# Performance work log

Hardware: AMD Instinct MI355X
Metric: run time of the kernel (lower is better)

The kernel has to match this reference:

```python
import jax, jax.numpy as jnp
import numpy as np

L, Q = 200, 21          # alignment length, number of Potts states (20 AAs + gap)
REG_H, REG_J = 0.01, 0.01  # L2 regularization strengths (reg_h, reg_J)
M = 1024                # number of sequences in the MSA


def setup_inputs() -> dict:
    key = jax.random.key(0)
    ks = jax.random.split(key, 6)
    X_tokens = jax.random.randint(ks[0], (M, L), 0, Q)
    weights = jax.random.uniform(ks[1], (M,), dtype=jnp.float32)
    fi = jax.random.uniform(ks[2], (L, Q), dtype=jnp.float32)
    fi_target = fi / fi.sum(axis=1, keepdims=True)  # single-site frequencies
    fij = jax.random.uniform(ks[3], (L, Q, L, Q), dtype=jnp.float32)
    fij_target = fij / fij.sum(axis=(1, 3), keepdims=True)  # pairwise frequencies
    h = jax.random.normal(ks[4], (L, Q), dtype=jnp.float32) * 1e-4
    J = jax.random.normal(ks[5], (L, Q, L, Q), dtype=jnp.float32) * 1e-4
    # remove_autocorr: zero self-couplings J[i,:,i,:]
    eye = jnp.eye(L, dtype=jnp.float32)[:, None, :, None]
    J = J * (1.0 - eye)
    return {"X_tokens": X_tokens, "weights": weights, "fi_target": fi_target,
            "fij_target": fij_target, "h": h, "J": J}


def _loss_third(X, weights, fi_target, fij_target, h, J):
    # loss_third_fn: sites i in [2L//3, L)
    start = 2 * L // 3
    w = weights / weights.sum()
    sites = jnp.arange(start, L)                         # (S,)
    causal = (jnp.arange(L)[None, :] < sites[:, None])   # (S, L), j < i mask
    Jm = J[start:] * causal[:, None, :, None].astype(J.dtype)  # (S, q, L, q)
    # energy_i = fi[i] @ h[i] + sum_{j<i} J[i,:,j,:] * fij[i,:,j,:], summed over i
    energy = (jnp.einsum('ia,ia->', fi_target[start:], h[start:])
              + jnp.einsum('iajb,iajb->', Jm, fij_target[start:]))
    # logits[n,i,a] = h[i,a] + sum_{j<i,b} J[i,a,j,b] * X[n,j,b]
    logits = jnp.einsum('njb,iajb->nia', X, Jm) + h[start:][None]  # (M, S, q)
    logZ = jax.scipy.special.logsumexp(logits, axis=-1)            # (M, S)
    nll = -(energy - jnp.einsum('ni,n->', logZ, w))
    loss = nll + REG_H * jnp.sum(h * h) + REG_J * jnp.sum(J * J)
    return loss, nll


def reference(X_tokens, weights, fi_target, fij_target, h, J):
    X = jax.nn.one_hot(X_tokens, Q, dtype=jnp.float32)  # (M, L, q)
    return _loss_third(X, weights, fi_target, fij_target, h, J)
```

## Files before the change

### kernel.cpp

```cpp
#include <hip/hip_runtime.h>
#include <cstdint>

#define LL    200
#define QQ    21
#define MM    1024
#define START 133
#define NS    67
#define RGH   0.01f
#define RGJ   0.01f

#define SLOT_J2  0
#define SLOT_E   64
#define SLOT_LZ  128
#define TOKT_OFF 1024
#define TOKT_BYTES ((size_t)LL * MM * 4)
#define SLAB_OFF (TOKT_OFF + TOKT_BYTES)
#define SLAB_BYTES ((size_t)2 * NS * QQ * MM * 4)
#define WS_FULL (SLAB_OFF + SLAB_BYTES)
#define WS_TOK  SLAB_OFF

#define TJ 12
#define PLANE 256
#define TILE_FLOATS (QQ * PLANE)

#define NB_P1 (NS * 8)
#define NB_JS 1024

typedef const uint32_t __attribute__((address_space(1)))* gq_t;
typedef uint32_t __attribute__((address_space(3)))* lq_t;

__device__ __forceinline__ float block_reduce_sum_256(float v) {
  __shared__ float sm[4];
  #pragma unroll
  for (int off = 32; off > 0; off >>= 1) v += __shfl_down(v, off, 64);
  const int lane = threadIdx.x & 63;
  const int wv   = threadIdx.x >> 6;
  __syncthreads();
  if (lane == 0) sm[wv] = v;
  __syncthreads();
  float r = 0.0f;
  if (threadIdx.x == 0) r = sm[0] + sm[1] + sm[2] + sm[3];
  return r;
}

__device__ __forceinline__ void dma_tile(
    const float* __restrict__ Ji, int j0, int rem, int wv, int lane,
    float* __restrict__ tile) {
  const int nlanes = (rem * QQ + 3) >> 2;
  if (lane < nlanes) {
    for (int a = wv; a < QQ; a += 4) {
      const float* g = Ji + a * (LL * QQ) + j0 * QQ + lane * 4;
      __builtin_amdgcn_global_load_lds((gq_t)g, (lq_t)(tile + a * PLANE),
                                       16, 0, 0);
    }
  }
}

__device__ __forceinline__ void tok_load(
    const int* __restrict__ tokT, const int* __restrict__ Xtok, int useT,
    int j0, int jend, int n, int (&bo)[TJ]) {
  #pragma unroll
  for (int k = 0; k < TJ; ++k) {
    if (j0 + k < jend) {
      const int j = j0 + k;
      const int b = useT ? tokT[j * MM + n] : Xtok[n * LL + j];
      bo[k] = k * QQ + b;
    }
  }
}

__device__ __forceinline__ void gather_tile(
    const float* __restrict__ tile, const int (&bo)[TJ], int rem,
    float (&lg)[QQ]) {
  #pragma unroll
  for (int jl = 0; jl < TJ; ++jl) {
    if (jl >= rem) break;
    const float* p = tile + bo[jl];
    #pragma unroll
    for (int a = 0; a < QQ; ++a) lg[a] += p[a * PLANE];
  }
}

template <bool MONO>
__device__ __forceinline__ void logz_body(
    const float* __restrict__ J, const int* __restrict__ tokT,
    const int* __restrict__ Xtok, int useT, const float* __restrict__ h,
    const float* __restrict__ w, float* __restrict__ slab,
    float* __restrict__ acc, int iI, int y, int z,
    float (*lds)[TILE_FLOATS]) {
  const int i  = START + iI;
  const int h0 = i >> 1;
  const int jbeg = MONO ? 0 : (y ? h0 : 0);
  const int jend = MONO ? i : (y ? i : h0);
  const int t = threadIdx.x, lane = t & 63, wv = t >> 6;
  const int n = z * 256 + t;
  const float* Ji = J + (size_t)i * (QQ * LL * QQ);
  const int ntiles = (jend - jbeg + TJ - 1) / TJ;

  float lg[QQ];
  #pragma unroll
  for (int a = 0; a < QQ; ++a) lg[a] = 0.0f;
  int boc[TJ], bon[TJ];

  dma_tile(Ji, jbeg, min(TJ, jend - jbeg), wv, lane, lds[0]);
  tok_load(tokT, Xtok, useT, jbeg, jend, n, boc);
  __syncthreads();

  for (int s = 0; s < ntiles; ++s) {
    const int j0  = jbeg + s * TJ;
    const int rem = min(TJ, jend - j0);
    const bool more = (s + 1 < ntiles);
    if (more) {
      const int j1 = j0 + TJ;
      dma_tile(Ji, j1, min(TJ, jend - j1), wv, lane, lds[(s + 1) & 1]);
      tok_load(tokT, Xtok, useT, j1, jend, n, bon);
    }
    gather_tile(lds[s & 1], boc, rem, lg);
    if (more) {
      #pragma unroll
      for (int k = 0; k < TJ; ++k) boc[k] = bon[k];
    }
    __syncthreads();
  }

  if (MONO) {
    const float* hi = h + i * QQ;
    float mx = -3.0e38f;
    #pragma unroll
    for (int a = 0; a < QQ; ++a) { lg[a] += hi[a]; mx = fmaxf(mx, lg[a]); }
    float sme = 0.0f;
    #pragma unroll
    for (int a = 0; a < QQ; ++a) sme += expf(lg[a] - mx);
    const float contrib = w[n] * (mx + logf(sme));
    const float tot = block_reduce_sum_256(contrib);
    if (t == 0) atomicAdd(acc + SLOT_LZ + (iI & 63), tot);
  } else {
    float* dst = slab + (((size_t)y * NS + iI) * QQ) * MM + n;
    #pragma unroll
    for (int a = 0; a < QQ; ++a) dst[a * MM] = lg[a];
  }
}

__device__ __forceinline__ void jsum_body(
    const float* __restrict__ J, const float* __restrict__ fij,
    float* __restrict__ acc, int jb) {
  const int t = threadIdx.x;
  const float4* __restrict__ J4 = (const float4*)J;
  float j2 = 0.0f;
  for (int f = jb * 256 + t; f < (LL * QQ * LL * QQ / 4); f += NB_JS * 256) {
    const float4 v = J4[f];
    j2 += v.x * v.x + v.y * v.y + v.z * v.z + v.w * v.w;
  }
  float e = 0.0f;
  for (int r = jb; r < NS * QQ; r += NB_JS) {
    const int iI = r / QQ;
    const int a  = r - iI * QQ;
    const int i  = START + iI;
    const size_t base = (size_t)i * (QQ * LL * QQ) + (size_t)a * (LL * QQ);
    const float4* __restrict__ Jb = (const float4*)(J + base);
    const float4* __restrict__ Fb = (const float4*)(fij + base);
    const int lim  = i * QQ;
    const int lim4 = lim >> 2;
    for (int f = t; f < lim4; f += 256) {
      const float4 v = Jb[f], u = Fb[f];
      e += v.x * u.x + v.y * u.y + v.z * u.z + v.w * u.w;
    }
    const int rem = lim & 3;
    if (t < rem) {
      const int p = lim4 * 4 + t;
      e += (J + base)[p] * (fij + base)[p];
    }
  }
  const float tj2 = block_reduce_sum_256(j2);
  const float te  = block_reduce_sum_256(e);
  if (t == 0) {
    atomicAdd(acc + SLOT_J2 + (jb & 63), tj2);
    atomicAdd(acc + SLOT_E  + (jb & 63), te);
  }
}

__global__ __launch_bounds__(256) void kern_mega(
    const float* __restrict__ J, const float* __restrict__ fij,
    const int* __restrict__ tokT, float* __restrict__ slab,
    float* __restrict__ acc) {
  __shared__ float lds[2][TILE_FLOATS];
  const int bx = blockIdx.x;
  if (bx < NB_P1) {
    const int iI  = bx % NS;
    const int sub = bx / NS;
    logz_body<false>(J, tokT, nullptr, 1, nullptr, nullptr, slab, acc,
                     iI, sub & 1, sub >> 1, lds);
  } else {
    jsum_body(J, fij, acc, bx - NB_P1);
  }
}

__global__ __launch_bounds__(256) void kern_logz_mono(
    const float* __restrict__ J, const int* __restrict__ tokT,
    const int* __restrict__ Xtok, int useT, const float* __restrict__ h,
    const float* __restrict__ w, float* __restrict__ acc) {
  __shared__ float lds[2][TILE_FLOATS];
  logz_body<true>(J, tokT, Xtok, useT, h, w, nullptr, acc,
                  blockIdx.x, 0, blockIdx.z, lds);
}

__global__ __launch_bounds__(256) void kern_jsum(
    const float* __restrict__ J, const float* __restrict__ fij,
    float* __restrict__ acc) {
  jsum_body(J, fij, acc, blockIdx.x);
}

__global__ __launch_bounds__(128) void kern_logz_p2(
    const float* __restrict__ slab, const float* __restrict__ h,
    const float* __restrict__ w, float* __restrict__ acc) {
  const int iI = blockIdx.x;
  const int n  = blockIdx.y * 128 + threadIdx.x;
  const float* s0 = slab + ((size_t)iI * QQ) * MM + n;
  const float* s1 = slab + (((size_t)NS + iI) * QQ) * MM + n;
  const float* hi = h + (START + iI) * QQ;
  float lg[QQ];
  float mx = -3.0e38f;
  #pragma unroll
  for (int a = 0; a < QQ; ++a) {
    lg[a] = s0[a * MM] + s1[a * MM] + hi[a];
    mx = fmaxf(mx, lg[a]);
  }
  float sme = 0.0f;
  #pragma unroll
  for (int a = 0; a < QQ; ++a) sme += expf(lg[a] - mx);
  float v = w[n] * (mx + logf(sme));
  #pragma unroll
  for (int off = 32; off > 0; off >>= 1) v += __shfl_down(v, off, 64);
  __shared__ float sm[2];
  if ((threadIdx.x & 63) == 0) sm[threadIdx.x >> 6] = v;
  __syncthreads();
  if (threadIdx.x == 0)
    atomicAdd(acc + SLOT_LZ + (blockIdx.x & 63), sm[0] + sm[1]);
}

__global__ __launch_bounds__(256) void kern_tokT(
    const int* __restrict__ X, int* __restrict__ tokT) {
  const int idx = blockIdx.x * 256 + threadIdx.x;
  if (idx < LL * MM) {
    const int j = idx / MM;
    const int n = idx - j * MM;
    tokT[idx] = X[n * LL + j];
  }
}

__global__ __launch_bounds__(256) void kern_final(
    const float* __restrict__ h, const float* __restrict__ fi,
    const float* __restrict__ w, const float* __restrict__ acc,
    float* __restrict__ out) {
  const int t = threadIdx.x;
  const float sj2 = block_reduce_sum_256(t < 64 ? acc[SLOT_J2 + t] : 0.0f);
  const float se  = block_reduce_sum_256(t < 64 ? acc[SLOT_E + t] : 0.0f);
  const float slz = block_reduce_sum_256(t < 64 ? acc[SLOT_LZ + t] : 0.0f);
  float hs = 0.0f, eh = 0.0f, ws = 0.0f;
  for (int idx = t; idx < LL * QQ; idx += 256) {
    const float hv = h[idx];
    hs += hv * hv;
    if (idx >= START * QQ) eh += fi[idx] * hv;
  }
  for (int idx = t; idx < MM; idx += 256) ws += w[idx];
  const float ths = block_reduce_sum_256(hs);
  const float teh = block_reduce_sum_256(eh);
  const float tws = block_reduce_sum_256(ws);
  if (t == 0) {
    const float energy = teh + se;
    const float nll = slz / tws - energy;
    out[0] = nll + RGH * ths + RGJ * sj2;
    out[1] = nll;
  }
}

extern "C" void kernel_launch(void* const* d_in, const int* in_sizes, int n_in,
                              void* d_out, int out_size, void* d_ws, size_t ws_size,
                              hipStream_t stream) {
  const int*   Xtok = (const int*)  d_in[0];
  const float* wts  = (const float*)d_in[1];
  const float* fi   = (const float*)d_in[2];
  const float* fij  = (const float*)d_in[3];
  const float* h    = (const float*)d_in[4];
  const float* J    = (const float*)d_in[5];
  float* out  = (float*)d_out;
  float* acc  = (float*)d_ws;
  int*   tokT = (int*)((char*)d_ws + TOKT_OFF);
  float* slab = (float*)((char*)d_ws + SLAB_OFF);

  hipMemsetAsync(d_ws, 0, 1024, stream);
  if (ws_size >= WS_FULL) {
    kern_tokT<<<(LL * MM + 255) / 256, 256, 0, stream>>>(Xtok, tokT);
    kern_mega<<<NB_P1 + NB_JS, 256, 0, stream>>>(J, fij, tokT, slab, acc);
    kern_logz_p2<<<dim3(NS, 8), 128, 0, stream>>>(slab, h, wts, acc);
    kern_final<<<1, 256, 0, stream>>>(h, fi, wts, acc, out);
  } else if (ws_size >= WS_TOK) {
    kern_tokT<<<(LL * MM + 255) / 256, 256, 0, stream>>>(Xtok, tokT);
    kern_jsum<<<NB_JS, 256, 0, stream>>>(J, fij, acc);
    kern_logz_mono<<<dim3(NS, 1, 4), 256, 0, stream>>>(J, tokT, Xtok, 1, h, wts, acc);
    kern_final<<<1, 256, 0, stream>>>(h, fi, wts, acc, out);
  } else {
    kern_jsum<<<NB_JS, 256, 0, stream>>>(J, fij, acc);
    kern_logz_mono<<<dim3(NS, 1, 4), 256, 0, stream>>>(J, nullptr, Xtok, 0, h, wts, acc);
    kern_final<<<1, 256, 0, stream>>>(h, fi, wts, acc, out);
  }
}
```

Measured before the change: 207.0 us.

## Fuse pipeline into persistent cooperative kernel with atomic work queue

Replaces the memset plus four separate launches with one cooperative persistent kernel. Inside it, blocks zero the accumulators and transpose the tokens, then pull logits and J-sum work units from an atomic counter, with the longest rows scheduled first; grid syncs separate this from the logsumexp reduction and the final reduction. It also shrinks the LDS tile (TJ 12 to 10, plane stride 256 to 212), makes the J² sweep read contiguous chunks per block, and widens the p2 blocks to 256 threads. The aim is to remove launch gaps and tail imbalance, at the cost of grid-wide sync overhead and a fixed grid size derived from the occupancy query.

```diff
diff --git a/kernel.cpp b/kernel.cpp
--- a/kernel.cpp
+++ b/kernel.cpp
@@ -1,5 +1,8 @@
 #include <hip/hip_runtime.h>
+#include <hip/hip_cooperative_groups.h>
 #include <cstdint>
+
+namespace cg = cooperative_groups;
 
 #define LL    200
 #define QQ    21
@@ -12,6 +15,7 @@
 #define SLOT_J2  0
 #define SLOT_E   64
 #define SLOT_LZ  128
+#define CTR_OFF  192
 #define TOKT_OFF 1024
 #define TOKT_BYTES ((size_t)LL * MM * 4)
 #define SLAB_OFF (TOKT_OFF + TOKT_BYTES)
@@ -19,12 +23,15 @@
 #define WS_FULL (SLAB_OFF + SLAB_BYTES)
 #define WS_TOK  SLAB_OFF
 
-#define TJ 12
-#define PLANE 256
+#define TJ 10
+#define PLANE 212
 #define TILE_FLOATS (QQ * PLANE)
 
-#define NB_P1 (NS * 8)
-#define NB_JS 1024
+#define NP1  (NS * 8)
+#define NJS  1024
+#define NTOT (NP1 + NJS)
+#define TOTAL4 (LL * QQ * LL * QQ / 4)
+#define CHUNK4 ((TOTAL4 + NJS - 1) / NJS)
 
 typedef const uint32_t __attribute__((address_space(1)))* gq_t;
 typedef uint32_t __attribute__((address_space(3)))* lq_t;
@@ -57,15 +64,10 @@
 }
 
 __device__ __forceinline__ void tok_load(
-    const int* __restrict__ tokT, const int* __restrict__ Xtok, int useT,
-    int j0, int jend, int n, int (&bo)[TJ]) {
+    const int* __restrict__ tokT, int j0, int jend, int n, int (&bo)[TJ]) {
   #pragma unroll
   for (int k = 0; k < TJ; ++k) {
-    if (j0 + k < jend) {
-      const int j = j0 + k;
-      const int b = useT ? tokT[j * MM + n] : Xtok[n * LL + j];
-      bo[k] = k * QQ + b;
-    }
+    if (j0 + k < jend) bo[k] = k * QQ + tokT[(j0 + k) * MM + n];
   }
 }
 
@@ -81,17 +83,14 @@
   }
 }
 
-template <bool MONO>
-__device__ __forceinline__ void logz_body(
+__device__ void p1_unit(
     const float* __restrict__ J, const int* __restrict__ tokT,
-    const int* __restrict__ Xtok, int useT, const float* __restrict__ h,
-    const float* __restrict__ w, float* __restrict__ slab,
-    float* __restrict__ acc, int iI, int y, int z,
+    float* __restrict__ slab, int iI, int y, int z,
     float (*lds)[TILE_FLOATS]) {
   const int i  = START + iI;
   const int h0 = i >> 1;
-  const int jbeg = MONO ? 0 : (y ? h0 : 0);
-  const int jend = MONO ? i : (y ? i : h0);
+  const int jbeg = y ? h0 : 0;
+  const int jend = y ? i : h0;
   const int t = threadIdx.x, lane = t & 63, wv = t >> 6;
   const int n = z * 256 + t;
   const float* Ji = J + (size_t)i * (QQ * LL * QQ);
@@ -103,7 +102,7 @@
   int boc[TJ], bon[TJ];
 
   dma_tile(Ji, jbeg, min(TJ, jend - jbeg), wv, lane, lds[0]);
-  tok_load(tokT, Xtok, useT, jbeg, jend, n, boc);
+  tok_load(tokT, jbeg, jend, n, boc);
   __syncthreads();
 
   for (int s = 0; s < ntiles; ++s) {
@@ -113,7 +112,7 @@
     if (more) {
       const int j1 = j0 + TJ;
       dma_tile(Ji, j1, min(TJ, jend - j1), wv, lane, lds[(s + 1) & 1]);
-      tok_load(tokT, Xtok, useT, j1, jend, n, bon);
+      tok_load(tokT, j1, jend, n, bon);
     }
     gather_tile(lds[s & 1], boc, rem, lg);
     if (more) {
@@ -123,36 +122,25 @@
     __syncthreads();
   }
 
-  if (MONO) {
-    const float* hi = h + i * QQ;
-    float mx = -3.0e38f;
-    #pragma unroll
-    for (int a = 0; a < QQ; ++a) { lg[a] += hi[a]; mx = fmaxf(mx, lg[a]); }
-    float sme = 0.0f;
-    #pragma unroll
-    for (int a = 0; a < QQ; ++a) sme += expf(lg[a] - mx);
-    const float contrib = w[n] * (mx + logf(sme));
-    const float tot = block_reduce_sum_256(contrib);
-    if (t == 0) atomicAdd(acc + SLOT_LZ + (iI & 63), tot);
-  } else {
-    float* dst = slab + (((size_t)y * NS + iI) * QQ) * MM + n;
-    #pragma unroll
-    for (int a = 0; a < QQ; ++a) dst[a * MM] = lg[a];
-  }
-}
-
-__device__ __forceinline__ void jsum_body(
+  float* dst = slab + (((size_t)y * NS + iI) * QQ) * MM + n;
+  #pragma unroll
+  for (int a = 0; a < QQ; ++a) dst[a * MM] = lg[a];
+}
+
+__device__ void jsum_unit(
     const float* __restrict__ J, const float* __restrict__ fij,
-    float* __restrict__ acc, int jb) {
+    float* __restrict__ acc, int v) {
   const int t = threadIdx.x;
   const float4* __restrict__ J4 = (const float4*)J;
   float j2 = 0.0f;
-  for (int f = jb * 256 + t; f < (LL * QQ * LL * QQ / 4); f += NB_JS * 256) {
-    const float4 v = J4[f];
-    j2 += v.x * v.x + v.y * v.y + v.z * v.z + v.w * v.w;
+  const int beg = v * CHUNK4;
+  const int end = min(beg + CHUNK4, TOTAL4);
+  for (int f = beg + t; f < end; f += 256) {
+    const float4 q = J4[f];
+    j2 += q.x * q.x + q.y * q.y + q.z * q.z + q.w * q.w;
   }
   float e = 0.0f;
-  for (int r = jb; r < NS * QQ; r += NB_JS) {
+  for (int r = v; r < NS * QQ; r += NJS) {
     const int iI = r / QQ;
     const int a  = r - iI * QQ;
     const int i  = START + iI;
@@ -162,8 +150,8 @@
     const int lim  = i * QQ;
     const int lim4 = lim >> 2;
     for (int f = t; f < lim4; f += 256) {
-      const float4 v = Jb[f], u = Fb[f];
-      e += v.x * u.x + v.y * u.y + v.z * u.z + v.w * u.w;
+      const float4 q = Jb[f], u = Fb[f];
+      e += q.x * u.x + q.y * u.y + q.z * u.z + q.w * u.w;
     }
     const int rem = lim & 3;
     if (t < rem) {
@@ -174,47 +162,16 @@
   const float tj2 = block_reduce_sum_256(j2);
   const float te  = block_reduce_sum_256(e);
   if (t == 0) {
-    atomicAdd(acc + SLOT_J2 + (jb & 63), tj2);
-    atomicAdd(acc + SLOT_E  + (jb & 63), te);
-  }
-}
-
-__global__ __launch_bounds__(256) void kern_mega(
-    const float* __restrict__ J, const float* __restrict__ fij,
-    const int* __restrict__ tokT, float* __restrict__ slab,
-    float* __restrict__ acc) {
-  __shared__ float lds[2][TILE_FLOATS];
-  const int bx = blockIdx.x;
-  if (bx < NB_P1) {
-    const int iI  = bx % NS;
-    const int sub = bx / NS;
-    logz_body<false>(J, tokT, nullptr, 1, nullptr, nullptr, slab, acc,
-                     iI, sub & 1, sub >> 1, lds);
-  } else {
-    jsum_body(J, fij, acc, bx - NB_P1);
-  }
-}
-
-__global__ __launch_bounds__(256) void kern_logz_mono(
-    const float* __restrict__ J, const int* __restrict__ tokT,
-    const int* __restrict__ Xtok, int useT, const float* __restrict__ h,
-    const float* __restrict__ w, float* __restrict__ acc) {
-  __shared__ float lds[2][TILE_FLOATS];
-  logz_body<true>(J, tokT, Xtok, useT, h, w, nullptr, acc,
-                  blockIdx.x, 0, blockIdx.z, lds);
-}
-
-__global__ __launch_bounds__(256) void kern_jsum(
-    const float* __restrict__ J, const float* __restrict__ fij,
-    float* __restrict__ acc) {
-  jsum_body(J, fij, acc, blockIdx.x);
-}
-
-__global__ __launch_bounds__(128) void kern_logz_p2(
+    atomicAdd(acc + SLOT_J2 + (v & 63), tj2);
+    atomicAdd(acc + SLOT_E  + (v & 63), te);
+  }
+}
+
+__device__ void p2_unit(
     const float* __restrict__ slab, const float* __restrict__ h,
-    const float* __restrict__ w, float* __restrict__ acc) {
-  const int iI = blockIdx.x;
-  const int n  = blockIdx.y * 128 + threadIdx.x;
+    const float* __restrict__ w, float* __restrict__ acc, int iI, int z) {
+  const int t = threadIdx.x;
+  const int n = z * 256 + t;
   const float* s0 = slab + ((size_t)iI * QQ) * MM + n;
   const float* s1 = slab + (((size_t)NS + iI) * QQ) * MM + n;
   const float* hi = h + (START + iI) * QQ;
@@ -228,27 +185,12 @@
   float sme = 0.0f;
   #pragma unroll
   for (int a = 0; a < QQ; ++a) sme += expf(lg[a] - mx);
-  float v = w[n] * (mx + logf(sme));
-  #pragma unroll
-  for (int off = 32; off > 0; off >>= 1) v += __shfl_down(v, off, 64);
-  __shared__ float sm[2];
-  if ((threadIdx.x & 63) == 0) sm[threadIdx.x >> 6] = v;
-  __syncthreads();
-  if (threadIdx.x == 0)
-    atomicAdd(acc + SLOT_LZ + (blockIdx.x & 63), sm[0] + sm[1]);
-}
-
-__global__ __launch_bounds__(256) void kern_tokT(
-    const int* __restrict__ X, int* __restrict__ tokT) {
-  const int idx = blockIdx.x * 256 + threadIdx.x;
-  if (idx < LL * MM) {
-    const int j = idx / MM;
-    const int n = idx - j * MM;
-    tokT[idx] = X[n * LL + j];
-  }
-}
-
-__global__ __launch_bounds__(256) void kern_final(
+  const float contrib = w[n] * (mx + logf(sme));
+  const float tot = block_reduce_sum_256(contrib);
+  if (t == 0) atomicAdd(acc + SLOT_LZ + (iI & 63), tot);
+}
+
+__device__ void final_body(
     const float* __restrict__ h, const float* __restrict__ fi,
     const float* __restrict__ w, const float* __restrict__ acc,
     float* __restrict__ out) {
@@ -272,6 +214,135 @@
     out[0] = nll + RGH * ths + RGJ * sj2;
     out[1] = nll;
   }
+}
+
+__global__ __launch_bounds__(256) void kern_coop(
+    const int* __restrict__ Xtok, const float* __restrict__ wts,
+    const float* __restrict__ fi, const float* __restrict__ fij,
+    const float* __restrict__ h, const float* __restrict__ J,
+    float* __restrict__ acc, int* __restrict__ tokT,
+    float* __restrict__ slab, float* __restrict__ out) {
+  __shared__ float lds[2][TILE_FLOATS];
+  __shared__ int s_unit;
+  cg::grid_group grid = cg::this_grid();
+  const int t = threadIdx.x;
+  const int nb = gridDim.x;
+
+  if (blockIdx.x == 0) acc[t] = 0.0f;
+  for (int idx = blockIdx.x * 256 + t; idx < LL * MM; idx += nb * 256) {
+    const int j = idx >> 10;
+    const int n = idx & (MM - 1);
+    tokT[idx] = Xtok[n * LL + j];
+  }
+  __threadfence();
+  grid.sync();
+
+  int* ctr = (int*)(acc + CTR_OFF);
+  for (;;) {
+    __syncthreads();
+    if (t == 0) s_unit = atomicAdd(ctr, 1);
+    __syncthreads();
+    const int u = s_unit;
+    if (u >= NTOT) break;
+    if (u < NP1) {
+      const int s    = u % NS;
+      const int rest = u / NS;
+      p1_unit(J, tokT, slab, NS - 1 - s, rest & 1, rest >> 1, lds);
+    } else {
+      jsum_unit(J, fij, acc, u - NP1);
+    }
+  }
+  __threadfence();
+  grid.sync();
+
+  for (int u = blockIdx.x; u < NS * 4; u += nb) {
+    p2_unit(slab, h, wts, acc, u >> 2, u & 3);
+  }
+  __threadfence();
+  grid.sync();
+
+  if (blockIdx.x == 0) final_body(h, fi, wts, acc, out);
+}
+
+__global__ __launch_bounds__(256) void kern_tokT(
+    const int* __restrict__ X, int* __restrict__ tokT) {
+  const int idx = blockIdx.x * 256 + threadIdx.x;
+  if (idx < LL * MM) tokT[idx] = X[(idx & (MM - 1)) * LL + (idx >> 10)];
+}
+
+__global__ __launch_bounds__(256) void kern_mega(
+    const float* __restrict__ J, const float* __restrict__ fij,
+    const int* __restrict__ tokT, float* __restrict__ slab,
+    float* __restrict__ acc) {
+  __shared__ float lds[2][TILE_FLOATS];
+  const int bx = blockIdx.x;
+  if (bx < NP1) {
+    const int s    = bx % NS;
+    const int rest = bx / NS;
+    p1_unit(J, tokT, slab, NS - 1 - s, rest & 1, rest >> 1, lds);
+  } else {
+    jsum_unit(J, fij, acc, bx - NP1);
+  }
+}
+
+__global__ __launch_bounds__(256) void kern_logz_p2(
+    const float* __restrict__ slab, const float* __restrict__ h,
+    const float* __restrict__ w, float* __restrict__ acc) {
+  p2_unit(slab, h, w, acc, blockIdx.x, blockIdx.y);
+}
+
+__global__ __launch_bounds__(256) void kern_final(
+    const float* __restrict__ h, const float* __restrict__ fi,
+    const float* __restrict__ w, const float* __restrict__ acc,
+    float* __restrict__ out) {
+  final_body(h, fi, w, acc, out);
+}
+
+__global__ __launch_bounds__(256) void kern_logz_mono(
+    const float* __restrict__ J, const int* __restrict__ Xtok,
+    const float* __restrict__ h, const float* __restrict__ w,
+    float* __restrict__ acc) {
+  __shared__ float lds[2][TILE_FLOATS];
+  const int i = START + blockIdx.x;
+  const int t = threadIdx.x, lane = t & 63, wv = t >> 6;
+  const int n = blockIdx.z * 256 + t;
+  const float* Ji = J + (size_t)i * (QQ * LL * QQ);
+  const int ntiles = (i + TJ - 1) / TJ;
+  float lg[QQ];
+  #pragma unroll
+  for (int a = 0; a < QQ; ++a) lg[a] = 0.0f;
+  int boc[TJ];
+  dma_tile(Ji, 0, min(TJ, i), wv, lane, lds[0]);
+  __syncthreads();
+  for (int s = 0; s < ntiles; ++s) {
+    const int j0  = s * TJ;
+    const int rem = min(TJ, i - j0);
+    #pragma unroll
+    for (int k = 0; k < TJ; ++k)
+      if (k < rem) boc[k] = k * QQ + Xtok[n * LL + (j0 + k)];
+    if (s + 1 < ntiles) {
+      const int j1 = j0 + TJ;
+      dma_tile(Ji, j1, min(TJ, i - j1), wv, lane, lds[(s + 1) & 1]);
+    }
+    gather_tile(lds[s & 1], boc, rem, lg);
+    __syncthreads();
+  }
+  const float* hi = h + i * QQ;
+  float mx = -3.0e38f;
+  #pragma unroll
+  for (int a = 0; a < QQ; ++a) { lg[a] += hi[a]; mx = fmaxf(mx, lg[a]); }
+  float sme = 0.0f;
+  #pragma unroll
+  for (int a = 0; a < QQ; ++a) sme += expf(lg[a] - mx);
+  const float contrib = w[n] * (mx + logf(sme));
+  const float tot = block_reduce_sum_256(contrib);
+  if (t == 0) atomicAdd(acc + SLOT_LZ + (blockIdx.x & 63), tot);
+}
+
+__global__ __launch_bounds__(256) void kern_jsum_only(
+    const float* __restrict__ J, const float* __restrict__ fij,
+    float* __restrict__ acc) {
+  jsum_unit(J, fij, acc, blockIdx.x);
 }
 
 extern "C" void kernel_launch(void* const* d_in, const int* in_sizes, int n_in,
@@ -288,20 +359,27 @@
   int*   tokT = (int*)((char*)d_ws + TOKT_OFF);
   float* slab = (float*)((char*)d_ws + SLAB_OFF);
 
-  hipMemsetAsync(d_ws, 0, 1024, stream);
   if (ws_size >= WS_FULL) {
+    int perCU = 0;
+    hipError_t qe = hipOccupancyMaxActiveBlocksPerMultiprocessor(
+        &perCU, (const void*)kern_coop, 256, 0);
+    int grid = (qe == hipSuccess && perCU > 0) ? perCU * 256 : 512;
+    if (grid > 1024) grid = 1024;
+    void* args[] = {(void*)&Xtok, (void*)&wts, (void*)&fi, (void*)&fij,
+                    (void*)&h,    (void*)&J,   (void*)&acc, (void*)&tokT,
+                    (void*)&slab, (void*)&out};
+    hipError_t le = hipLaunchCooperativeKernel(
+        (const void*)kern_coop, dim3(grid), dim3(256), args, 0, stream);
+    if (le == hipSuccess) return;
+    hipMemsetAsync(d_ws, 0, 1024, stream);
     kern_tokT<<<(LL * MM + 255) / 256, 256, 0, stream>>>(Xtok, tokT);
-    kern_mega<<<NB_P1 + NB_JS, 256, 0, stream>>>(J, fij, tokT, slab, acc);
-    kern_logz_p2<<<dim3(NS, 8), 128, 0, stream>>>(slab, h, wts, acc);
-    kern_final<<<1, 256, 0, stream>>>(h, fi, wts, acc, out);
-  } else if (ws_size >= WS_TOK) {
-    kern_tokT<<<(LL * MM + 255) / 256, 256, 0, stream>>>(Xtok, tokT);
-    kern_jsum<<<NB_JS, 256, 0, stream>>>(J, fij, acc);
-    kern_logz_mono<<<dim3(NS, 1, 4), 256, 0, stream>>>(J, tokT, Xtok, 1, h, wts, acc);
+    kern_mega<<<NP1 + NJS, 256, 0, stream>>>(J, fij, tokT, slab, acc);
+    kern_logz_p2<<<dim3(NS, 4), 256, 0, stream>>>(slab, h, wts, acc);
     kern_final<<<1, 256, 0, stream>>>(h, fi, wts, acc, out);
   } else {
-    kern_jsum<<<NB_JS, 256, 0, stream>>>(J, fij, acc);
-    kern_logz_mono<<<dim3(NS, 1, 4), 256, 0, stream>>>(J, nullptr, Xtok, 0, h, wts, acc);
+    hipMemsetAsync(d_ws, 0, 1024, stream);
+    kern_jsum_only<<<NJS, 256, 0, stream>>>(J, fij, acc);
+    kern_logz_mono<<<dim3(NS, 1, 4), 256, 0, stream>>>(J, Xtok, h, wts, acc);
     kern_final<<<1, 256, 0, stream>>>(h, fi, wts, acc, out);
   }
 }
```

After: 602.1 us. +190.9%, slower.
